# Performance work log

Measured on AMD Instinct MI355X. Metric: run time of the kernel, lower is better.

Reference implementation:

```python
import jax, jax.numpy as jnp
import numpy as np

# Cost coefficients from MatcherConfig (init_kwargs)
C_CLASS, C_MASK, C_DICE, C_DIST, C_NLL, C_LIK = 2.0, 5.0, 5.0, 1.0, 0.5, 0.5

B, P, Q, E = 8, 16384, 256, 128  # images, pixels (H*W), queries, electrons


def setup_inputs() -> dict:
    key = jax.random.key(0)
    ks = jax.random.split(key, 8)
    mask_mask = jax.random.uniform(ks[0], (B, P, Q)) < 0.10           # sparsity pattern of pred logits
    mask_logit_values = jax.random.normal(ks[1], (B, P, Q), jnp.float32)
    seg_occ = jax.random.uniform(ks[2], (B, P, E)) < 0.05              # sparsity pattern of target segmap
    seg_vals = jax.random.uniform(ks[3], (B, P, E), jnp.float32, 1e-3, 1.0)
    segmap_values = jnp.where(seg_occ, seg_vals, 0.0)
    pred_logits = jax.random.normal(ks[4], (B, Q), jnp.float32)
    pred_positions = jax.random.uniform(ks[5], (B, Q, 2), jnp.float32)
    true_positions = jax.random.uniform(ks[6], (B, E, 2), jnp.float32)
    kd, ko = jax.random.split(ks[7])
    diag = 1.0 + 2.0 * jax.random.uniform(kd, (B, Q, 2), jnp.float32)  # positive diag of scale_tril
    off = 0.3 * jax.random.normal(ko, (B, Q), jnp.float32)
    pred_chol = jnp.zeros((B, Q, 2, 2), jnp.float32)
    pred_chol = pred_chol.at[..., 0, 0].set(diag[..., 0])
    pred_chol = pred_chol.at[..., 1, 1].set(diag[..., 1])
    pred_chol = pred_chol.at[..., 1, 0].set(off)
    image_sizes_xy = jnp.full((B, 2), 128.0, jnp.float32)
    return {
        'pred_logits': pred_logits,
        'mask_logit_values': mask_logit_values,
        'mask_mask': mask_mask,
        'segmap_values': segmap_values,
        'pred_positions': pred_positions,
        'pred_chol': pred_chol,
        'true_positions': true_positions,
        'image_sizes_xy': image_sizes_xy,
    }


def _total_cost(pred_logits, mask_logit_values, segmap_values, pred_positions,
                pred_chol, true_positions, image_sizes_xy, mask_mask):
    sp = jax.nn.softplus
    m = mask_mask
    # --- class cost: BCE(logit, 1) per query -> [B,Q]
    class_cost = sp(-pred_logits)
    # --- mask BCE cost (get_bce_cost): sparse entries only
    pos = jnp.where(m, sp(-mask_logit_values), 0.0)   # BCE vs 1 on nnz entries
    neg = jnp.where(m, sp(mask_logit_values), 0.0)    # BCE vs 0 on nnz entries
    targ = (segmap_values > 0).astype(pos.dtype)      # binarized target segmap
    pos_loss = jnp.einsum('bpq,bpe->bqe', pos, targ)
    neg_loss = neg.sum(1)[:, :, None] - jnp.einsum('bpq,bpe->bqe', neg, targ)
    nnz = jnp.maximum(targ.sum((1, 2)), 1.0)          # target _nnz() per image
    mask_cost = (pos_loss + neg_loss) / nnz[:, None, None]
    # --- dice cost (get_dice_cost): sparse softmax over query dim
    NEG = jnp.asarray(-1e30, mask_logit_values.dtype)
    z = jnp.where(m, mask_logit_values, NEG)
    mx = jnp.max(z, axis=-1, keepdims=True)
    ez = jnp.where(m, jnp.exp(z - mx), 0.0)
    s = ez.sum(-1, keepdims=True)
    pred_p = jnp.where(s > 0, ez / jnp.maximum(s, 1e-30), 0.0)  # [B,P,Q]
    num = 2.0 * jnp.einsum('bpq,bpe->bqe', pred_p, segmap_values)
    den = pred_p.sum(1)[:, :, None] + segmap_values.sum(1)[:, None, :]
    dice_cost = 1.0 - (num + 1.0) / (den + 1.0)
    # --- huber distance cost (delta=1), mean over xy
    d = pred_positions[:, :, None, :] - true_positions[:, None, :, :]  # [B,Q,E,2]
    ad = jnp.abs(d)
    huber_cost = jnp.where(ad < 1.0, 0.5 * d * d, ad - 0.5).mean(-1)
    # --- NLL / likelihood distance costs (MVN with scale_tril)
    mu = pred_positions * image_sizes_xy[:, None, :]
    y = true_positions * image_sizes_xy[:, None, :]
    diff = y[:, None, :, :] - mu[:, :, None, :]        # [B,Q,E,2]
    L00 = pred_chol[..., 0, 0][:, :, None]
    L10 = pred_chol[..., 1, 0][:, :, None]
    L11 = pred_chol[..., 1, 1][:, :, None]
    z0 = diff[..., 0] / L00
    z1 = (diff[..., 1] - L10 * z0) / L11
    nll_cost = 0.5 * (z0 * z0 + z1 * z1) + jnp.log(2.0 * jnp.pi) + jnp.log(L00) + jnp.log(L11)
    lik_cost = 1.0 - jnp.exp(-nll_cost)
    total = (C_CLASS * class_cost[:, :, None] + C_MASK * mask_cost + C_DICE * dice_cost
             + C_DIST * huber_cost + C_NLL * nll_cost + C_LIK * lik_cost)
    return total  # [B, Q, E] stacked per-image cost matrices


def reference(pred_logits, mask_logit_values, mask_mask, segmap_values,
              pred_positions, pred_chol, true_positions, image_sizes_xy):
    return _total_cost(pred_logits, mask_logit_values, segmap_values, pred_positions,
                       pred_chol, true_positions, image_sizes_xy, mask_mask)
```

## Files before the change

### kernel.cpp

```cpp
#include <hip/hip_runtime.h>
#include <cstdint>
#include <cstddef>

typedef float v4f __attribute__((ext_vector_type(4)));
typedef short short8 __attribute__((ext_vector_type(8)));

constexpr int B_ = 8, P_ = 16384, Q_ = 256, E_ = 128;

__device__ __forceinline__ unsigned int f2bf(float f) {
  unsigned int x = __float_as_uint(f);
  x += 0x7FFFu + ((x >> 16) & 1u);
  return x >> 16;
}
__device__ __forceinline__ float softplus_f(float x) {
  return fmaxf(x, 0.f) + __logf(1.f + __expf(-fabsf(x)));
}
__device__ __forceinline__ short8 mk8(unsigned a, unsigned b, unsigned c, unsigned d) {
  union { unsigned u[4]; short8 s; } x;
  x.u[0] = a; x.u[1] = b; x.u[2] = c; x.u[3] = d; return x.s;
}
__device__ __forceinline__ float wsum(float v) {
#pragma unroll
  for (int o = 32; o; o >>= 1) v += __shfl_xor(v, o, 64);
  return v;
}

__device__ __forceinline__ void lds_barrier() {
  asm volatile("s_waitcnt lgkmcnt(0)" ::: "memory");
  __builtin_amdgcn_s_barrier();
}

__global__ __launch_bounds__(512, 2) void fused_all(
    const float* __restrict__ mlv, const int* __restrict__ mask,
    const float* __restrict__ seg, float* __restrict__ part,
    float* __restrict__ negsum, float* __restrict__ ppsum,
    float* __restrict__ segsum, float* __restrict__ nnzb)
{
  __shared__ __align__(16) unsigned int lds[12544];
  unsigned int* A1t = lds;
  unsigned int* EZt = lds + 4160;
  unsigned int* SBt = lds + 8320;
  unsigned int* STt = lds + 10432;

  const int t = threadIdx.x, w = t >> 6, l = t & 63;
  const int lm = l & 15, quad = l >> 4;
  const int wr = w & 3, wc = w >> 2;
  const int jj = l >> 5, le = l & 31;
  const int b = blockIdx.x >> 5, ks = blockIdx.x & 31;

  v4f acc0[4][4], acc1[4][4];
#pragma unroll
  for (int i = 0; i < 4; ++i)
#pragma unroll
    for (int j = 0; j < 4; ++j) { acc0[i][j] = (v4f)0.f; acc1[i][j] = (v4f)0.f; }
  float accN[4] = {0.f,0.f,0.f,0.f};
  float accP[4] = {0.f,0.f,0.f,0.f};
  float accS[4] = {0.f,0.f,0.f,0.f};
  float cnt = 0.f;

  const float* mp = mlv + ((size_t)b * P_ + ks * 512 + 4 * w) * Q_ + 4 * l;
  const int*   kp = mask + ((size_t)b * P_ + ks * 512 + 4 * w) * Q_ + 4 * l;
  const float* sp = seg + ((size_t)b * P_ + ks * 512 + 4 * w + 2 * jj) * E_ + 4 * le;

  float4 X[4]; int4 M[4]; float4 S0, S1;
#pragma unroll
  for (int r = 0; r < 4; ++r) {
    X[r] = *(const float4*)(mp + (size_t)r * Q_);
    M[r] = *(const int4*)(kp + (size_t)r * Q_);
  }
  S0 = *(const float4*)(sp);
  S1 = *(const float4*)(sp + E_);

  for (int it = 0; it < 16; ++it) {
    float xs[4][4]; int ms[4][4];
#pragma unroll
    for (int r = 0; r < 4; ++r) {
      xs[r][0] = X[r].x; xs[r][1] = X[r].y; xs[r][2] = X[r].z; xs[r][3] = X[r].w;
      ms[r][0] = M[r].x; ms[r][1] = M[r].y; ms[r][2] = M[r].z; ms[r][3] = M[r].w;
    }
    float sv0[4] = {S0.x, S0.y, S0.z, S0.w};
    float sv1[4] = {S1.x, S1.y, S1.z, S1.w};

    if (it < 15) {
      mp += 32 * Q_; kp += 32 * Q_; sp += 32 * E_;
#pragma unroll
      for (int r = 0; r < 4; ++r) {
        X[r] = *(const float4*)(mp + (size_t)r * Q_);
        M[r] = *(const int4*)(kp + (size_t)r * Q_);
      }
      S0 = *(const float4*)(sp);
      S1 = *(const float4*)(sp + E_);
    }

    float ez[4][4], rs[4];
#pragma unroll
    for (int r = 0; r < 4; ++r) {
      float s = 0.f;
#pragma unroll
      for (int j = 0; j < 4; ++j) {
        const bool mm = ms[r][j] != 0;
        const float e = mm ? __expf(xs[r][j]) : 0.f;
        ez[r][j] = e; s += e;
        accN[j] += __logf(1.f + e);
      }
      rs[r] = s;
    }
#pragma unroll
    for (int r = 0; r < 4; ++r) rs[r] = wsum(rs[r]);
    float inv[4];
#pragma unroll
    for (int r = 0; r < 4; ++r) inv[r] = (rs[r] > 0.f) ? (1.f / rs[r]) : 0.f;

    unsigned int a1p[2][4], ezp[2][4];
#pragma unroll
    for (int jp = 0; jp < 2; ++jp)
#pragma unroll
      for (int j = 0; j < 4; ++j) {
        const int r0 = 2 * jp, r1 = 2 * jp + 1;
        a1p[jp][j] = f2bf(ms[r0][j] ? -xs[r0][j] : 0.f)
                   | (f2bf(ms[r1][j] ? -xs[r1][j] : 0.f) << 16);
        const float p0 = ez[r0][j] * inv[r0];
        const float p1 = ez[r1][j] * inv[r1];
        accP[j] += p0 + p1;
        ezp[jp][j] = f2bf(p0) | (f2bf(p1) << 16);
      }
    unsigned int sb[4], st_[4];
#pragma unroll
    for (int j = 0; j < 4; ++j) {
      accS[j] += sv0[j] + sv1[j];
      cnt += ((sv0[j] > 0.f) ? 1.f : 0.f) + ((sv1[j] > 0.f) ? 1.f : 0.f);
      sb[j]  = ((sv0[j] > 0.f) ? 0x3F80u : 0u) | ((sv1[j] > 0.f) ? 0x3F800000u : 0u);
      st_[j] = f2bf(sv0[j]) | (f2bf(sv1[j]) << 16);
    }

    lds_barrier();
    { uint4 v; v.x=a1p[0][0]; v.y=a1p[0][1]; v.z=a1p[0][2]; v.w=a1p[0][3];
      *(uint4*)(A1t + (2*w)     * 260 + 4*l) = v; }
    { uint4 v; v.x=a1p[1][0]; v.y=a1p[1][1]; v.z=a1p[1][2]; v.w=a1p[1][3];
      *(uint4*)(A1t + (2*w + 1) * 260 + 4*l) = v; }
    { uint4 v; v.x=ezp[0][0]; v.y=ezp[0][1]; v.z=ezp[0][2]; v.w=ezp[0][3];
      *(uint4*)(EZt + (2*w)     * 260 + 4*l) = v; }
    { uint4 v; v.x=ezp[1][0]; v.y=ezp[1][1]; v.z=ezp[1][2]; v.w=ezp[1][3];
      *(uint4*)(EZt + (2*w + 1) * 260 + 4*l) = v; }
    { uint4 v; v.x=sb[0]; v.y=sb[1]; v.z=sb[2]; v.w=sb[3];
      *(uint4*)(SBt + (2*w + jj) * 132 + 4*le) = v; }
    { uint4 v; v.x=st_[0]; v.y=st_[1]; v.z=st_[2]; v.w=st_[3];
      *(uint4*)(STt + (2*w + jj) * 132 + 4*le) = v; }
    lds_barrier();

    short8 af0[4], af1[4], bf0[4], bf1[4];
#pragma unroll
    for (int i = 0; i < 4; ++i) {
      const int q_abs = wr * 64 + i * 16 + lm;
      const int c0 = 4 * quad;
      af0[i] = mk8(A1t[c0*260 + q_abs], A1t[(c0+1)*260 + q_abs],
                   A1t[(c0+2)*260 + q_abs], A1t[(c0+3)*260 + q_abs]);
      af1[i] = mk8(EZt[c0*260 + q_abs], EZt[(c0+1)*260 + q_abs],
                   EZt[(c0+2)*260 + q_abs], EZt[(c0+3)*260 + q_abs]);
    }
#pragma unroll
    for (int j = 0; j < 4; ++j) {
      const int e_abs = wc * 64 + j * 16 + lm;
      const int c0 = 4 * quad;
      bf0[j] = mk8(SBt[c0*132 + e_abs], SBt[(c0+1)*132 + e_abs],
                   SBt[(c0+2)*132 + e_abs], SBt[(c0+3)*132 + e_abs]);
      bf1[j] = mk8(STt[c0*132 + e_abs], STt[(c0+1)*132 + e_abs],
                   STt[(c0+2)*132 + e_abs], STt[(c0+3)*132 + e_abs]);
    }
#pragma unroll
    for (int i = 0; i < 4; ++i)
#pragma unroll
      for (int j = 0; j < 4; ++j) {
        acc0[i][j] = __builtin_amdgcn_mfma_f32_16x16x32_bf16(af0[i], bf0[j], acc0[i][j], 0, 0, 0);
        acc1[i][j] = __builtin_amdgcn_mfma_f32_16x16x32_bf16(af1[i], bf1[j], acc1[i][j], 0, 0, 0);
      }
  }

  __syncthreads();
  float* fr = (float*)lds;
#pragma unroll
  for (int j = 0; j < 4; ++j) {
    fr[w * 256 + 4 * l + j] = accN[j];
    fr[2048 + w * 256 + 4 * l + j] = accP[j];
    fr[4096 + (2 * w + jj) * 128 + 4 * le + j] = accS[j];
  }
  __syncthreads();
  if (t < 256) {
    float sn = 0.f, sq = 0.f;
#pragma unroll
    for (int k = 0; k < 8; ++k) { sn += fr[k * 256 + t]; sq += fr[2048 + k * 256 + t]; }
    atomicAdd(&negsum[b * 256 + t], sn);
    atomicAdd(&ppsum[b * 256 + t], sq);
  } else if (t < 384) {
    const int e = t - 256;
    float ss = 0.f;
#pragma unroll
    for (int k = 0; k < 16; ++k) ss += fr[4096 + k * 128 + e];
    atomicAdd(&segsum[b * 128 + e], ss);
  }
  cnt = wsum(cnt);
  if (l == 0) atomicAdd(&nnzb[b], cnt);

  float* p0 = part + (size_t)b * 32768;
  float* p1 = part + (size_t)(8 + b) * 32768;
#pragma unroll
  for (int i = 0; i < 4; ++i)
#pragma unroll
    for (int r = 0; r < 4; ++r) {
      const int q = wr * 64 + i * 16 + quad * 4 + r;
#pragma unroll
      for (int j = 0; j < 4; ++j) {
        const int e = wc * 64 + j * 16 + lm;
        atomicAdd(&p0[q * 128 + e], acc0[i][j][r]);
        atomicAdd(&p1[q * 128 + e], acc1[i][j][r]);
      }
    }
}

__global__ __launch_bounds__(128) void epilogue(
    const float* __restrict__ part,
    const float* __restrict__ negsum, const float* __restrict__ ppsum,
    const float* __restrict__ segsum, const float* __restrict__ nnzb,
    const float* __restrict__ logits, const float* __restrict__ ppos,
    const float* __restrict__ chol, const float* __restrict__ tpos,
    const float* __restrict__ imgsz, float* __restrict__ out)
{
  const int bq = blockIdx.x;
  const int b = bq >> 8;
  const int e = threadIdx.x;
  const int qe = (bq & 255) * 128 + e;
  const float g1 = part[(size_t)b * 32768 + qe];
  const float g2 = part[(size_t)(8 + b) * 32768 + qe];

  const float nnz = fmaxf(nnzb[b], 1.f);
  const float mask_cost = (negsum[bq] + g1) / nnz;
  const float dice = 1.f - (2.f * g2 + 1.f) / (ppsum[bq] + segsum[b * 128 + e] + 1.f);
  const float cls = softplus_f(-logits[bq]);
  const float px = ppos[bq * 2], py = ppos[bq * 2 + 1];
  const float tx = tpos[(b * 128 + e) * 2], ty = tpos[(b * 128 + e) * 2 + 1];
  const float dx = px - tx, dy = py - ty;
  const float ax = fabsf(dx), ay = fabsf(dy);
  const float hx = (ax < 1.f) ? 0.5f * dx * dx : ax - 0.5f;
  const float hy = (ay < 1.f) ? 0.5f * dy * dy : ay - 0.5f;
  const float huber = 0.5f * (hx + hy);
  const float sx = imgsz[b * 2], sy = imgsz[b * 2 + 1];
  const float L00 = chol[bq * 4 + 0], L10 = chol[bq * 4 + 2], L11 = chol[bq * 4 + 3];
  const float d0 = (tx - px) * sx, d1 = (ty - py) * sy;
  const float z0 = d0 / L00;
  const float z1 = (d1 - L10 * z0) / L11;
  const float nll = 0.5f * (z0 * z0 + z1 * z1) + 1.8378770664093453f + __logf(L00) + __logf(L11);
  const float lik = 1.f - __expf(-nll);
  out[bq * 128 + e] = 2.f * cls + 5.f * mask_cost + 5.f * dice + huber + 0.5f * nll + 0.5f * lik;
}

extern "C" void kernel_launch(void* const* d_in, const int* in_sizes, int n_in,
                              void* d_out, int out_size, void* d_ws, size_t ws_size,
                              hipStream_t stream)
{
  (void)in_sizes; (void)n_in; (void)out_size; (void)ws_size;
  const float* logits = (const float*)d_in[0];
  const float* mlv    = (const float*)d_in[1];
  const int*   mask   = (const int*)d_in[2];
  const float* seg    = (const float*)d_in[3];
  const float* ppos   = (const float*)d_in[4];
  const float* chol   = (const float*)d_in[5];
  const float* tpos   = (const float*)d_in[6];
  const float* imgsz  = (const float*)d_in[7];

  char* ws = (char*)d_ws;
  float* part   = (float*)(ws);
  float* negsum = (float*)(ws + 2097152);
  float* ppsum  = (float*)(ws + 2105344);
  float* segsum = (float*)(ws + 2113536);
  float* nnzb   = (float*)(ws + 2117632);

  hipMemsetAsync(ws, 0, 2117664, stream);
  fused_all<<<256, 512, 0, stream>>>(mlv, mask, seg, part, negsum, ppsum, segsum, nnzb);
  epilogue<<<2048, 128, 0, stream>>>(part, negsum, ppsum, segsum, nnzb,
                                     logits, ppos, chol, tpos, imgsz, (float*)d_out);
}
```

Before: 416.2 us.

## Write per-split partials directly, double-buffer LDS, interleave prefetch with compute

Each block now writes its GEMM partial tiles to a private slice of a 64MB workspace with plain stores, and the epilogue reduces the 32 split-K slices. This replaces the global float atomics and the 2MB memset. LDS is double-buffered by iteration parity, which removes the barrier before the writes, and the per-row prefetch loads are spread across the compute stages. The cost is 64MB of extra partial traffic written and re-read by the epilogue, plus twice the shared memory. The old atomic path remains as a fallback when the workspace is too small.

```diff
diff --git a/kernel.cpp b/kernel.cpp
--- a/kernel.cpp
+++ b/kernel.cpp
@@ -24,24 +24,19 @@
   for (int o = 32; o; o >>= 1) v += __shfl_xor(v, o, 64);
   return v;
 }
-
 __device__ __forceinline__ void lds_barrier() {
   asm volatile("s_waitcnt lgkmcnt(0)" ::: "memory");
   __builtin_amdgcn_s_barrier();
 }
 
+template<bool DIRECT>
 __global__ __launch_bounds__(512, 2) void fused_all(
     const float* __restrict__ mlv, const int* __restrict__ mask,
     const float* __restrict__ seg, float* __restrict__ part,
     float* __restrict__ negsum, float* __restrict__ ppsum,
     float* __restrict__ segsum, float* __restrict__ nnzb)
 {
-  __shared__ __align__(16) unsigned int lds[12544];
-  unsigned int* A1t = lds;
-  unsigned int* EZt = lds + 4160;
-  unsigned int* SBt = lds + 8320;
-  unsigned int* STt = lds + 10432;
-
+  __shared__ __align__(16) unsigned int lds[25088];
   const int t = threadIdx.x, w = t >> 6, l = t & 63;
   const int lm = l & 15, quad = l >> 4;
   const int wr = w & 3, wc = w >> 2;
@@ -63,89 +58,114 @@
   const float* sp = seg + ((size_t)b * P_ + ks * 512 + 4 * w + 2 * jj) * E_ + 4 * le;
 
   float4 X[4]; int4 M[4]; float4 S0, S1;
-#pragma unroll
-  for (int r = 0; r < 4; ++r) {
-    X[r] = *(const float4*)(mp + (size_t)r * Q_);
-    M[r] = *(const int4*)(kp + (size_t)r * Q_);
-  }
-  S0 = *(const float4*)(sp);
-  S1 = *(const float4*)(sp + E_);
-
+  X[0] = *(const float4*)(mp);           M[0] = *(const int4*)(kp);
+  X[1] = *(const float4*)(mp + Q_);      M[1] = *(const int4*)(kp + Q_);
+  X[2] = *(const float4*)(mp + 2 * Q_);  M[2] = *(const int4*)(kp + 2 * Q_);
+  X[3] = *(const float4*)(mp + 3 * Q_);  M[3] = *(const int4*)(kp + 3 * Q_);
+  S0 = *(const float4*)(sp);             S1 = *(const float4*)(sp + E_);
+
+#pragma unroll 2
   for (int it = 0; it < 16; ++it) {
-    float xs[4][4]; int ms[4][4];
-#pragma unroll
-    for (int r = 0; r < 4; ++r) {
-      xs[r][0] = X[r].x; xs[r][1] = X[r].y; xs[r][2] = X[r].z; xs[r][3] = X[r].w;
-      ms[r][0] = M[r].x; ms[r][1] = M[r].y; ms[r][2] = M[r].z; ms[r][3] = M[r].w;
-    }
-    float sv0[4] = {S0.x, S0.y, S0.z, S0.w};
-    float sv1[4] = {S1.x, S1.y, S1.z, S1.w};
-
-    if (it < 15) {
-      mp += 32 * Q_; kp += 32 * Q_; sp += 32 * E_;
-#pragma unroll
-      for (int r = 0; r < 4; ++r) {
-        X[r] = *(const float4*)(mp + (size_t)r * Q_);
-        M[r] = *(const int4*)(kp + (size_t)r * Q_);
-      }
-      S0 = *(const float4*)(sp);
-      S1 = *(const float4*)(sp + E_);
-    }
-
-    float ez[4][4], rs[4];
-#pragma unroll
-    for (int r = 0; r < 4; ++r) {
-      float s = 0.f;
-#pragma unroll
-      for (int j = 0; j < 4; ++j) {
-        const bool mm = ms[r][j] != 0;
-        const float e = mm ? __expf(xs[r][j]) : 0.f;
-        ez[r][j] = e; s += e;
-        accN[j] += __logf(1.f + e);
-      }
-      rs[r] = s;
-    }
-#pragma unroll
-    for (int r = 0; r < 4; ++r) rs[r] = wsum(rs[r]);
-    float inv[4];
-#pragma unroll
-    for (int r = 0; r < 4; ++r) inv[r] = (rs[r] > 0.f) ? (1.f / rs[r]) : 0.f;
-
-    unsigned int a1p[2][4], ezp[2][4];
-#pragma unroll
-    for (int jp = 0; jp < 2; ++jp)
-#pragma unroll
-      for (int j = 0; j < 4; ++j) {
-        const int r0 = 2 * jp, r1 = 2 * jp + 1;
-        a1p[jp][j] = f2bf(ms[r0][j] ? -xs[r0][j] : 0.f)
-                   | (f2bf(ms[r1][j] ? -xs[r1][j] : 0.f) << 16);
-        const float p0 = ez[r0][j] * inv[r0];
-        const float p1 = ez[r1][j] * inv[r1];
+    unsigned int* L  = lds + (it & 1) * 12544;
+    unsigned int* A1 = L;
+    unsigned int* EZ = L + 4160;
+    unsigned int* SB = L + 8320;
+    unsigned int* ST = L + 10432;
+    const float* mp2 = mp + 32 * Q_;
+    const int*   kp2 = kp + 32 * Q_;
+    const float* sp2 = sp + 32 * E_;
+    const bool pf = (it < 15);
+
+    {
+      float xs0[4] = {X[0].x, X[0].y, X[0].z, X[0].w};
+      int   ms0[4] = {M[0].x, M[0].y, M[0].z, M[0].w};
+      float xs1[4] = {X[1].x, X[1].y, X[1].z, X[1].w};
+      int   ms1[4] = {M[1].x, M[1].y, M[1].z, M[1].w};
+      if (pf) {
+        X[0] = *(const float4*)(mp2);       M[0] = *(const int4*)(kp2);
+        X[1] = *(const float4*)(mp2 + Q_);  M[1] = *(const int4*)(kp2 + Q_);
+      }
+      float ez0[4], ez1[4], s0 = 0.f, s1 = 0.f;
+#pragma unroll
+      for (int j = 0; j < 4; ++j) {
+        const float e0 = ms0[j] ? __expf(xs0[j]) : 0.f;
+        const float e1 = ms1[j] ? __expf(xs1[j]) : 0.f;
+        ez0[j] = e0; ez1[j] = e1; s0 += e0; s1 += e1;
+        accN[j] += __logf(1.f + e0) + __logf(1.f + e1);
+      }
+      s0 = wsum(s0); s1 = wsum(s1);
+      const float i0 = (s0 > 0.f) ? 1.f / s0 : 0.f;
+      const float i1 = (s1 > 0.f) ? 1.f / s1 : 0.f;
+      unsigned a_[4], e_[4];
+#pragma unroll
+      for (int j = 0; j < 4; ++j) {
+        a_[j] = f2bf(ms0[j] ? -xs0[j] : 0.f) | (f2bf(ms1[j] ? -xs1[j] : 0.f) << 16);
+        const float p0 = ez0[j] * i0, p1 = ez1[j] * i1;
         accP[j] += p0 + p1;
-        ezp[jp][j] = f2bf(p0) | (f2bf(p1) << 16);
-      }
-    unsigned int sb[4], st_[4];
-#pragma unroll
-    for (int j = 0; j < 4; ++j) {
-      accS[j] += sv0[j] + sv1[j];
-      cnt += ((sv0[j] > 0.f) ? 1.f : 0.f) + ((sv1[j] > 0.f) ? 1.f : 0.f);
-      sb[j]  = ((sv0[j] > 0.f) ? 0x3F80u : 0u) | ((sv1[j] > 0.f) ? 0x3F800000u : 0u);
-      st_[j] = f2bf(sv0[j]) | (f2bf(sv1[j]) << 16);
-    }
-
-    lds_barrier();
-    { uint4 v; v.x=a1p[0][0]; v.y=a1p[0][1]; v.z=a1p[0][2]; v.w=a1p[0][3];
-      *(uint4*)(A1t + (2*w)     * 260 + 4*l) = v; }
-    { uint4 v; v.x=a1p[1][0]; v.y=a1p[1][1]; v.z=a1p[1][2]; v.w=a1p[1][3];
-      *(uint4*)(A1t + (2*w + 1) * 260 + 4*l) = v; }
-    { uint4 v; v.x=ezp[0][0]; v.y=ezp[0][1]; v.z=ezp[0][2]; v.w=ezp[0][3];
-      *(uint4*)(EZt + (2*w)     * 260 + 4*l) = v; }
-    { uint4 v; v.x=ezp[1][0]; v.y=ezp[1][1]; v.z=ezp[1][2]; v.w=ezp[1][3];
-      *(uint4*)(EZt + (2*w + 1) * 260 + 4*l) = v; }
-    { uint4 v; v.x=sb[0]; v.y=sb[1]; v.z=sb[2]; v.w=sb[3];
-      *(uint4*)(SBt + (2*w + jj) * 132 + 4*le) = v; }
-    { uint4 v; v.x=st_[0]; v.y=st_[1]; v.z=st_[2]; v.w=st_[3];
-      *(uint4*)(STt + (2*w + jj) * 132 + 4*le) = v; }
+        e_[j] = f2bf(p0) | (f2bf(p1) << 16);
+      }
+      { uint4 v; v.x=a_[0]; v.y=a_[1]; v.z=a_[2]; v.w=a_[3];
+        *(uint4*)(A1 + (2*w) * 260 + 4*l) = v; }
+      { uint4 v; v.x=e_[0]; v.y=e_[1]; v.z=e_[2]; v.w=e_[3];
+        *(uint4*)(EZ + (2*w) * 260 + 4*l) = v; }
+    }
+
+    {
+      float xs0[4] = {X[2].x, X[2].y, X[2].z, X[2].w};
+      int   ms0[4] = {M[2].x, M[2].y, M[2].z, M[2].w};
+      float xs1[4] = {X[3].x, X[3].y, X[3].z, X[3].w};
+      int   ms1[4] = {M[3].x, M[3].y, M[3].z, M[3].w};
+      if (pf) {
+        X[2] = *(const float4*)(mp2 + 2 * Q_);  M[2] = *(const int4*)(kp2 + 2 * Q_);
+        X[3] = *(const float4*)(mp2 + 3 * Q_);  M[3] = *(const int4*)(kp2 + 3 * Q_);
+      }
+      float ez0[4], ez1[4], s0 = 0.f, s1 = 0.f;
+#pragma unroll
+      for (int j = 0; j < 4; ++j) {
+        const float e0 = ms0[j] ? __expf(xs0[j]) : 0.f;
+        const float e1 = ms1[j] ? __expf(xs1[j]) : 0.f;
+        ez0[j] = e0; ez1[j] = e1; s0 += e0; s1 += e1;
+        accN[j] += __logf(1.f + e0) + __logf(1.f + e1);
+      }
+      s0 = wsum(s0); s1 = wsum(s1);
+      const float i0 = (s0 > 0.f) ? 1.f / s0 : 0.f;
+      const float i1 = (s1 > 0.f) ? 1.f / s1 : 0.f;
+      unsigned a_[4], e_[4];
+#pragma unroll
+      for (int j = 0; j < 4; ++j) {
+        a_[j] = f2bf(ms0[j] ? -xs0[j] : 0.f) | (f2bf(ms1[j] ? -xs1[j] : 0.f) << 16);
+        const float p0 = ez0[j] * i0, p1 = ez1[j] * i1;
+        accP[j] += p0 + p1;
+        e_[j] = f2bf(p0) | (f2bf(p1) << 16);
+      }
+      { uint4 v; v.x=a_[0]; v.y=a_[1]; v.z=a_[2]; v.w=a_[3];
+        *(uint4*)(A1 + (2*w + 1) * 260 + 4*l) = v; }
+      { uint4 v; v.x=e_[0]; v.y=e_[1]; v.z=e_[2]; v.w=e_[3];
+        *(uint4*)(EZ + (2*w + 1) * 260 + 4*l) = v; }
+    }
+
+    {
+      float sv0[4] = {S0.x, S0.y, S0.z, S0.w};
+      float sv1[4] = {S1.x, S1.y, S1.z, S1.w};
+      if (pf) {
+        S0 = *(const float4*)(sp2);
+        S1 = *(const float4*)(sp2 + E_);
+      }
+      unsigned sb[4], st_[4];
+#pragma unroll
+      for (int j = 0; j < 4; ++j) {
+        accS[j] += sv0[j] + sv1[j];
+        cnt += ((sv0[j] > 0.f) ? 1.f : 0.f) + ((sv1[j] > 0.f) ? 1.f : 0.f);
+        sb[j]  = ((sv0[j] > 0.f) ? 0x3F80u : 0u) | ((sv1[j] > 0.f) ? 0x3F800000u : 0u);
+        st_[j] = f2bf(sv0[j]) | (f2bf(sv1[j]) << 16);
+      }
+      { uint4 v; v.x=sb[0]; v.y=sb[1]; v.z=sb[2]; v.w=sb[3];
+        *(uint4*)(SB + (2*w + jj) * 132 + 4*le) = v; }
+      { uint4 v; v.x=st_[0]; v.y=st_[1]; v.z=st_[2]; v.w=st_[3];
+        *(uint4*)(ST + (2*w + jj) * 132 + 4*le) = v; }
+    }
+    if (pf) { mp = mp2; kp = kp2; sp = sp2; }
+
     lds_barrier();
 
     short8 af0[4], af1[4], bf0[4], bf1[4];
@@ -153,19 +173,19 @@
     for (int i = 0; i < 4; ++i) {
       const int q_abs = wr * 64 + i * 16 + lm;
       const int c0 = 4 * quad;
-      af0[i] = mk8(A1t[c0*260 + q_abs], A1t[(c0+1)*260 + q_abs],
-                   A1t[(c0+2)*260 + q_abs], A1t[(c0+3)*260 + q_abs]);
-      af1[i] = mk8(EZt[c0*260 + q_abs], EZt[(c0+1)*260 + q_abs],
-                   EZt[(c0+2)*260 + q_abs], EZt[(c0+3)*260 + q_abs]);
+      af0[i] = mk8(A1[c0*260 + q_abs], A1[(c0+1)*260 + q_abs],
+                   A1[(c0+2)*260 + q_abs], A1[(c0+3)*260 + q_abs]);
+      af1[i] = mk8(EZ[c0*260 + q_abs], EZ[(c0+1)*260 + q_abs],
+                   EZ[(c0+2)*260 + q_abs], EZ[(c0+3)*260 + q_abs]);
     }
 #pragma unroll
     for (int j = 0; j < 4; ++j) {
       const int e_abs = wc * 64 + j * 16 + lm;
       const int c0 = 4 * quad;
-      bf0[j] = mk8(SBt[c0*132 + e_abs], SBt[(c0+1)*132 + e_abs],
-                   SBt[(c0+2)*132 + e_abs], SBt[(c0+3)*132 + e_abs]);
-      bf1[j] = mk8(STt[c0*132 + e_abs], STt[(c0+1)*132 + e_abs],
-                   STt[(c0+2)*132 + e_abs], STt[(c0+3)*132 + e_abs]);
+      bf0[j] = mk8(SB[c0*132 + e_abs], SB[(c0+1)*132 + e_abs],
+                   SB[(c0+2)*132 + e_abs], SB[(c0+3)*132 + e_abs]);
+      bf1[j] = mk8(ST[c0*132 + e_abs], ST[(c0+1)*132 + e_abs],
+                   ST[(c0+2)*132 + e_abs], ST[(c0+3)*132 + e_abs]);
     }
 #pragma unroll
     for (int i = 0; i < 4; ++i)
@@ -201,22 +221,40 @@
   cnt = wsum(cnt);
   if (l == 0) atomicAdd(&nnzb[b], cnt);
 
-  float* p0 = part + (size_t)b * 32768;
-  float* p1 = part + (size_t)(8 + b) * 32768;
-#pragma unroll
-  for (int i = 0; i < 4; ++i)
-#pragma unroll
-    for (int r = 0; r < 4; ++r) {
-      const int q = wr * 64 + i * 16 + quad * 4 + r;
-#pragma unroll
-      for (int j = 0; j < 4; ++j) {
-        const int e = wc * 64 + j * 16 + lm;
-        atomicAdd(&p0[q * 128 + e], acc0[i][j][r]);
-        atomicAdd(&p1[q * 128 + e], acc1[i][j][r]);
-      }
-    }
-}
-
+  if constexpr (DIRECT) {
+    float* p0 = part + ((size_t)(ks * 8 + b) * 2) * 32768;
+    float* p1 = p0 + 32768;
+#pragma unroll
+    for (int i = 0; i < 4; ++i)
+#pragma unroll
+      for (int r = 0; r < 4; ++r) {
+        const int q = wr * 64 + i * 16 + quad * 4 + r;
+#pragma unroll
+        for (int j = 0; j < 4; ++j) {
+          const int e = wc * 64 + j * 16 + lm;
+          p0[q * 128 + e] = acc0[i][j][r];
+          p1[q * 128 + e] = acc1[i][j][r];
+        }
+      }
+  } else {
+    float* p0 = part + (size_t)b * 32768;
+    float* p1 = part + (size_t)(8 + b) * 32768;
+#pragma unroll
+    for (int i = 0; i < 4; ++i)
+#pragma unroll
+      for (int r = 0; r < 4; ++r) {
+        const int q = wr * 64 + i * 16 + quad * 4 + r;
+#pragma unroll
+        for (int j = 0; j < 4; ++j) {
+          const int e = wc * 64 + j * 16 + lm;
+          atomicAdd(&p0[q * 128 + e], acc0[i][j][r]);
+          atomicAdd(&p1[q * 128 + e], acc1[i][j][r]);
+        }
+      }
+  }
+}
+
+template<bool DIRECT>
 __global__ __launch_bounds__(128) void epilogue(
     const float* __restrict__ part,
     const float* __restrict__ negsum, const float* __restrict__ ppsum,
@@ -229,8 +267,19 @@
   const int b = bq >> 8;
   const int e = threadIdx.x;
   const int qe = (bq & 255) * 128 + e;
-  const float g1 = part[(size_t)b * 32768 + qe];
-  const float g2 = part[(size_t)(8 + b) * 32768 + qe];
+
+  float g1, g2;
+  if constexpr (DIRECT) {
+    g1 = 0.f; g2 = 0.f;
+#pragma unroll 8
+    for (int ksi = 0; ksi < 32; ++ksi) {
+      g1 += part[((size_t)(ksi * 8 + b) * 2) * 32768 + qe];
+      g2 += part[((size_t)(ksi * 8 + b) * 2 + 1) * 32768 + qe];
+    }
+  } else {
+    g1 = part[(size_t)b * 32768 + qe];
+    g2 = part[(size_t)(8 + b) * 32768 + qe];
+  }
 
   const float nnz = fmaxf(nnzb[b], 1.f);
   const float mask_cost = (negsum[bq] + g1) / nnz;
@@ -257,7 +306,7 @@
                               void* d_out, int out_size, void* d_ws, size_t ws_size,
                               hipStream_t stream)
 {
-  (void)in_sizes; (void)n_in; (void)out_size; (void)ws_size;
+  (void)in_sizes; (void)n_in; (void)out_size;
   const float* logits = (const float*)d_in[0];
   const float* mlv    = (const float*)d_in[1];
   const int*   mask   = (const int*)d_in[2];
@@ -268,14 +317,28 @@
   const float* imgsz  = (const float*)d_in[7];
 
   char* ws = (char*)d_ws;
-  float* part   = (float*)(ws);
-  float* negsum = (float*)(ws + 2097152);
-  float* ppsum  = (float*)(ws + 2105344);
-  float* segsum = (float*)(ws + 2113536);
-  float* nnzb   = (float*)(ws + 2117632);
-
-  hipMemsetAsync(ws, 0, 2117664, stream);
-  fused_all<<<256, 512, 0, stream>>>(mlv, mask, seg, part, negsum, ppsum, segsum, nnzb);
-  epilogue<<<2048, 128, 0, stream>>>(part, negsum, ppsum, segsum, nnzb,
-                                     logits, ppos, chol, tpos, imgsz, (float*)d_out);
-}
+  const size_t PART_DIRECT = 67108864ull;
+  const size_t NEED = PART_DIRECT + 20512ull;
+
+  if (ws_size >= NEED) {
+    float* part   = (float*)ws;
+    float* negsum = (float*)(ws + PART_DIRECT);
+    float* ppsum  = (float*)(ws + PART_DIRECT + 8192);
+    float* segsum = (float*)(ws + PART_DIRECT + 16384);
+    float* nnzb   = (float*)(ws + PART_DIRECT + 20480);
+    hipMemsetAsync(ws + PART_DIRECT, 0, 20512, stream);
+    fused_all<true><<<256, 512, 0, stream>>>(mlv, mask, seg, part, negsum, ppsum, segsum, nnzb);
+    epilogue<true><<<2048, 128, 0, stream>>>(part, negsum, ppsum, segsum, nnzb,
+                                             logits, ppos, chol, tpos, imgsz, (float*)d_out);
+  } else {
+    float* part   = (float*)(ws);
+    float* negsum = (float*)(ws + 2097152);
+    float* ppsum  = (float*)(ws + 2105344);
+    float* segsum = (float*)(ws + 2113536);
+    float* nnzb   = (float*)(ws + 2117632);
+    hipMemsetAsync(ws, 0, 2117664, stream);
+    fused_all<false><<<256, 512, 0, stream>>>(mlv, mask, seg, part, negsum, ppsum, segsum, nnzb);
+    epilogue<false><<<2048, 128, 0, stream>>>(part, negsum, ppsum, segsum, nnzb,
+                                              logits, ppos, chol, tpos, imgsz, (float*)d_out);
+  }
+}
```

Result: slower. 559.7 us (+34.5%).

## Replace atomic split-K reduction with per-slice partial buffers and swizzle LDS operand layout

Applied to the files above, without the earlier changes.

When the workspace is large enough, each of the 32 K-slices writes its GEMM partials to its own buffer with plain stores. The epilogue then sums all 32 slices, replacing 2M global float atomics per batch-plane. The LDS staging layout is also changed to a k-contiguous XOR-swizzled form, so MFMA operands load as single 128-bit reads instead of four scalar reads. The cost is a 64 MB partial buffer that must be written and read back, and a fallback path is kept when the workspace is too small.

```diff
diff --git a/kernel.cpp b/kernel.cpp
--- a/kernel.cpp
+++ b/kernel.cpp
@@ -15,32 +15,31 @@
 __device__ __forceinline__ float softplus_f(float x) {
   return fmaxf(x, 0.f) + __logf(1.f + __expf(-fabsf(x)));
 }
-__device__ __forceinline__ short8 mk8(unsigned a, unsigned b, unsigned c, unsigned d) {
-  union { unsigned u[4]; short8 s; } x;
-  x.u[0] = a; x.u[1] = b; x.u[2] = c; x.u[3] = d; return x.s;
-}
 __device__ __forceinline__ float wsum(float v) {
 #pragma unroll
   for (int o = 32; o; o >>= 1) v += __shfl_xor(v, o, 64);
   return v;
 }
-
 __device__ __forceinline__ void lds_barrier() {
   asm volatile("s_waitcnt lgkmcnt(0)" ::: "memory");
   __builtin_amdgcn_s_barrier();
 }
-
+__device__ __forceinline__ int swz(int q, int kp) {
+  return ((q << 4) | kp) ^ (((q >> 3) & 7) << 2);
+}
+
+template<bool DIRECT>
 __global__ __launch_bounds__(512, 2) void fused_all(
     const float* __restrict__ mlv, const int* __restrict__ mask,
     const float* __restrict__ seg, float* __restrict__ part,
     float* __restrict__ negsum, float* __restrict__ ppsum,
     float* __restrict__ segsum, float* __restrict__ nnzb)
 {
-  __shared__ __align__(16) unsigned int lds[12544];
-  unsigned int* A1t = lds;
-  unsigned int* EZt = lds + 4160;
-  unsigned int* SBt = lds + 8320;
-  unsigned int* STt = lds + 10432;
+  __shared__ __align__(16) unsigned int lds[12288];
+  unsigned int* A1q = lds;
+  unsigned int* EZq = lds + 4096;
+  unsigned int* SBq = lds + 8192;
+  unsigned int* STq = lds + 10240;
 
   const int t = threadIdx.x, w = t >> 6, l = t & 63;
   const int lm = l & 15, quad = l >> 4;
@@ -134,38 +133,38 @@
     }
 
     lds_barrier();
-    { uint4 v; v.x=a1p[0][0]; v.y=a1p[0][1]; v.z=a1p[0][2]; v.w=a1p[0][3];
-      *(uint4*)(A1t + (2*w)     * 260 + 4*l) = v; }
-    { uint4 v; v.x=a1p[1][0]; v.y=a1p[1][1]; v.z=a1p[1][2]; v.w=a1p[1][3];
-      *(uint4*)(A1t + (2*w + 1) * 260 + 4*l) = v; }
-    { uint4 v; v.x=ezp[0][0]; v.y=ezp[0][1]; v.z=ezp[0][2]; v.w=ezp[0][3];
-      *(uint4*)(EZt + (2*w)     * 260 + 4*l) = v; }
-    { uint4 v; v.x=ezp[1][0]; v.y=ezp[1][1]; v.z=ezp[1][2]; v.w=ezp[1][3];
-      *(uint4*)(EZt + (2*w + 1) * 260 + 4*l) = v; }
-    { uint4 v; v.x=sb[0]; v.y=sb[1]; v.z=sb[2]; v.w=sb[3];
-      *(uint4*)(SBt + (2*w + jj) * 132 + 4*le) = v; }
-    { uint4 v; v.x=st_[0]; v.y=st_[1]; v.z=st_[2]; v.w=st_[3];
-      *(uint4*)(STt + (2*w + jj) * 132 + 4*le) = v; }
+#pragma unroll
+    for (int j = 0; j < 4; ++j) {
+      const int q = 4 * l + j;
+      const int wa = swz(q, 2 * w);
+      uint2 va; va.x = a1p[0][j]; va.y = a1p[1][j];
+      uint2 ve; ve.x = ezp[0][j]; ve.y = ezp[1][j];
+      *(uint2*)(A1q + wa) = va;
+      *(uint2*)(EZq + wa) = ve;
+    }
+#pragma unroll
+    for (int j = 0; j < 4; ++j) {
+      const int e = 4 * le + j;
+      const int wb = swz(e, 2 * w + jj);
+      SBq[wb] = sb[j];
+      STq[wb] = st_[j];
+    }
     lds_barrier();
 
     short8 af0[4], af1[4], bf0[4], bf1[4];
 #pragma unroll
     for (int i = 0; i < 4; ++i) {
       const int q_abs = wr * 64 + i * 16 + lm;
-      const int c0 = 4 * quad;
-      af0[i] = mk8(A1t[c0*260 + q_abs], A1t[(c0+1)*260 + q_abs],
-                   A1t[(c0+2)*260 + q_abs], A1t[(c0+3)*260 + q_abs]);
-      af1[i] = mk8(EZt[c0*260 + q_abs], EZt[(c0+1)*260 + q_abs],
-                   EZt[(c0+2)*260 + q_abs], EZt[(c0+3)*260 + q_abs]);
+      const int wa = swz(q_abs, 4 * quad);
+      af0[i] = *(const short8*)(A1q + wa);
+      af1[i] = *(const short8*)(EZq + wa);
     }
 #pragma unroll
     for (int j = 0; j < 4; ++j) {
       const int e_abs = wc * 64 + j * 16 + lm;
-      const int c0 = 4 * quad;
-      bf0[j] = mk8(SBt[c0*132 + e_abs], SBt[(c0+1)*132 + e_abs],
-                   SBt[(c0+2)*132 + e_abs], SBt[(c0+3)*132 + e_abs]);
-      bf1[j] = mk8(STt[c0*132 + e_abs], STt[(c0+1)*132 + e_abs],
-                   STt[(c0+2)*132 + e_abs], STt[(c0+3)*132 + e_abs]);
+      const int wb = swz(e_abs, 4 * quad);
+      bf0[j] = *(const short8*)(SBq + wb);
+      bf1[j] = *(const short8*)(STq + wb);
     }
 #pragma unroll
     for (int i = 0; i < 4; ++i)
@@ -201,22 +200,40 @@
   cnt = wsum(cnt);
   if (l == 0) atomicAdd(&nnzb[b], cnt);
 
-  float* p0 = part + (size_t)b * 32768;
-  float* p1 = part + (size_t)(8 + b) * 32768;
-#pragma unroll
-  for (int i = 0; i < 4; ++i)
-#pragma unroll
-    for (int r = 0; r < 4; ++r) {
-      const int q = wr * 64 + i * 16 + quad * 4 + r;
-#pragma unroll
-      for (int j = 0; j < 4; ++j) {
-        const int e = wc * 64 + j * 16 + lm;
-        atomicAdd(&p0[q * 128 + e], acc0[i][j][r]);
-        atomicAdd(&p1[q * 128 + e], acc1[i][j][r]);
-      }
-    }
-}
-
+  if constexpr (DIRECT) {
+    float* p0 = part + ((size_t)(ks * 8 + b) * 2) * 32768;
+    float* p1 = p0 + 32768;
+#pragma unroll
+    for (int i = 0; i < 4; ++i)
+#pragma unroll
+      for (int r = 0; r < 4; ++r) {
+        const int q = wr * 64 + i * 16 + quad * 4 + r;
+#pragma unroll
+        for (int j = 0; j < 4; ++j) {
+          const int e = wc * 64 + j * 16 + lm;
+          p0[q * 128 + e] = acc0[i][j][r];
+          p1[q * 128 + e] = acc1[i][j][r];
+        }
+      }
+  } else {
+    float* p0 = part + (size_t)b * 32768;
+    float* p1 = part + (size_t)(8 + b) * 32768;
+#pragma unroll
+    for (int i = 0; i < 4; ++i)
+#pragma unroll
+      for (int r = 0; r < 4; ++r) {
+        const int q = wr * 64 + i * 16 + quad * 4 + r;
+#pragma unroll
+        for (int j = 0; j < 4; ++j) {
+          const int e = wc * 64 + j * 16 + lm;
+          atomicAdd(&p0[q * 128 + e], acc0[i][j][r]);
+          atomicAdd(&p1[q * 128 + e], acc1[i][j][r]);
+        }
+      }
+  }
+}
+
+template<bool DIRECT>
 __global__ __launch_bounds__(128) void epilogue(
     const float* __restrict__ part,
     const float* __restrict__ negsum, const float* __restrict__ ppsum,
@@ -229,8 +246,19 @@
   const int b = bq >> 8;
   const int e = threadIdx.x;
   const int qe = (bq & 255) * 128 + e;
-  const float g1 = part[(size_t)b * 32768 + qe];
-  const float g2 = part[(size_t)(8 + b) * 32768 + qe];
+
+  float g1, g2;
+  if constexpr (DIRECT) {
+    g1 = 0.f; g2 = 0.f;
+#pragma unroll 8
+    for (int ksi = 0; ksi < 32; ++ksi) {
+      g1 += part[((size_t)(ksi * 8 + b) * 2) * 32768 + qe];
+      g2 += part[((size_t)(ksi * 8 + b) * 2 + 1) * 32768 + qe];
+    }
+  } else {
+    g1 = part[(size_t)b * 32768 + qe];
+    g2 = part[(size_t)(8 + b) * 32768 + qe];
+  }
 
   const float nnz = fmaxf(nnzb[b], 1.f);
   const float mask_cost = (negsum[bq] + g1) / nnz;
@@ -257,7 +285,7 @@
                               void* d_out, int out_size, void* d_ws, size_t ws_size,
                               hipStream_t stream)
 {
-  (void)in_sizes; (void)n_in; (void)out_size; (void)ws_size;
+  (void)in_sizes; (void)n_in; (void)out_size;
   const float* logits = (const float*)d_in[0];
   const float* mlv    = (const float*)d_in[1];
   const int*   mask   = (const int*)d_in[2];
@@ -268,14 +296,28 @@
   const float* imgsz  = (const float*)d_in[7];
 
   char* ws = (char*)d_ws;
-  float* part   = (float*)(ws);
-  float* negsum = (float*)(ws + 2097152);
-  float* ppsum  = (float*)(ws + 2105344);
-  float* segsum = (float*)(ws + 2113536);
-  float* nnzb   = (float*)(ws + 2117632);
-
-  hipMemsetAsync(ws, 0, 2117664, stream);
-  fused_all<<<256, 512, 0, stream>>>(mlv, mask, seg, part, negsum, ppsum, segsum, nnzb);
-  epilogue<<<2048, 128, 0, stream>>>(part, negsum, ppsum, segsum, nnzb,
-                                     logits, ppos, chol, tpos, imgsz, (float*)d_out);
-}
+  const size_t PART_DIRECT = 67108864ull;
+  const size_t NEED = PART_DIRECT + 20512ull;
+
+  if (ws_size >= NEED) {
+    float* part   = (float*)ws;
+    float* negsum = (float*)(ws + PART_DIRECT);
+    float* ppsum  = (float*)(ws + PART_DIRECT + 8192);
+    float* segsum = (float*)(ws + PART_DIRECT + 16384);
+    float* nnzb   = (float*)(ws + PART_DIRECT + 20480);
+    hipMemsetAsync(ws + PART_DIRECT, 0, 20512, stream);
+    fused_all<true><<<256, 512, 0, stream>>>(mlv, mask, seg, part, negsum, ppsum, segsum, nnzb);
+    epilogue<true><<<2048, 128, 0, stream>>>(part, negsum, ppsum, segsum, nnzb,
+                                             logits, ppos, chol, tpos, imgsz, (float*)d_out);
+  } else {
+    float* part   = (float*)(ws);
+    float* negsum = (float*)(ws + 2097152);
+    float* ppsum  = (float*)(ws + 2105344);
+    float* segsum = (float*)(ws + 2113536);
+    float* nnzb   = (float*)(ws + 2117632);
+    hipMemsetAsync(ws, 0, 2117664, stream);
+    fused_all<false><<<256, 512, 0, stream>>>(mlv, mask, seg, part, negsum, ppsum, segsum, nnzb);
+    epilogue<false><<<2048, 128, 0, stream>>>(part, negsum, ppsum, segsum, nnzb,
+                                              logits, ppos, chol, tpos, imgsz, (float*)d_out);
+  }
+}
```

After: 421.0 us. About the same (+1.2%).
